# Kernel tuning notes

Measured on AMD Instinct MI355X. Metric: run time of the kernel, lower is better.

## Reference

```python
import jax, jax.numpy as jnp
import numpy as np

X_DIM, Y_DIM = 5, 2
H1, H2 = 560, 40
GRU_H = 5 * (X_DIM * X_DIM + Y_DIM * Y_DIM)  # 145
N_GRU = 2


def _gru_cell(x, h, Wih, Whh, bih, bhh):
    # PyTorch GRUCell math. Wih:(3H,in), Whh:(3H,H)
    gi = Wih @ x + bih
    gh = Whh @ h + bhh
    i_r, i_z, i_n = jnp.split(gi, 3)
    h_r, h_z, h_n = jnp.split(gh, 3)
    r = jax.nn.sigmoid(i_r + h_r)
    z = jax.nn.sigmoid(i_z + h_z)
    n = jnp.tanh(i_n + r * h_n)
    return (1.0 - z) * n + z * h


def setup_inputs() -> dict:
    key = jax.random.key(0)
    ks = jax.random.split(key, 20)
    s = lambda k, sh, fan: (jax.random.uniform(k, sh, jnp.float32, -1.0, 1.0) / np.sqrt(fan))
    inp = {
        "state_inno": jax.random.normal(ks[0], (X_DIM,), jnp.float32),
        "obs_inno": jax.random.normal(ks[1], (Y_DIM,), jnp.float32),
        "diff_state": jax.random.normal(ks[2], (X_DIM,), jnp.float32),
        "diff_obs": jax.random.normal(ks[3], (Y_DIM,), jnp.float32),
        # l1: Linear(14 -> H1)
        "W1": s(ks[4], (H1, 2 * X_DIM + 2 * Y_DIM), 2 * X_DIM + 2 * Y_DIM),
        "b1": s(ks[5], (H1,), 2 * X_DIM + 2 * Y_DIM),
        # GRU layer 0: input H1 -> GRU_H
        "Wih0": s(ks[6], (3 * GRU_H, H1), GRU_H),
        "Whh0": s(ks[7], (3 * GRU_H, GRU_H), GRU_H),
        "bih0": s(ks[8], (3 * GRU_H,), GRU_H),
        "bhh0": s(ks[9], (3 * GRU_H,), GRU_H),
        # GRU layer 1: input GRU_H -> GRU_H
        "Wih1": s(ks[10], (3 * GRU_H, GRU_H), GRU_H),
        "Whh1": s(ks[11], (3 * GRU_H, GRU_H), GRU_H),
        "bih1": s(ks[12], (3 * GRU_H,), GRU_H),
        "bhh1": s(ks[13], (3 * GRU_H,), GRU_H),
        # l2: Linear(GRU_H -> H2) -> ReLU -> Linear(H2 -> x_dim*y_dim)
        "W2a": s(ks[14], (H2, GRU_H), GRU_H),
        "b2a": s(ks[15], (H2,), GRU_H),
        "W2b": s(ks[16], (X_DIM * Y_DIM, H2), H2),
        "b2b": s(ks[17], (X_DIM * Y_DIM,), H2),
        # hidden state hn: (n_layers, batch=1, GRU_H) -> squeeze batch
        "hn": jax.random.normal(ks[18], (N_GRU, GRU_H), jnp.float32),
    }
    return inp


def reference(state_inno, obs_inno, diff_state, diff_obs,
              W1, b1, Wih0, Whh0, bih0, bhh0, Wih1, Whh1, bih1, bhh1,
              W2a, b2a, W2b, b2b, hn):
    x = jnp.concatenate([state_inno, obs_inno, diff_state, diff_obs])  # (14,)
    l1_out = jax.nn.relu(W1 @ x + b1)  # (H1,)
    h0 = _gru_cell(l1_out, hn[0], Wih0, Whh0, bih0, bhh0)  # (GRU_H,)
    h1 = _gru_cell(h0, hn[1], Wih1, Whh1, bih1, bhh1)       # (GRU_H,)
    l2_hidden = jax.nn.relu(W2a @ h1 + b2a)
    l2_out = W2b @ l2_hidden + b2b  # (x_dim*y_dim,)
    kalman_gain = l2_out.reshape(X_DIM, Y_DIM)
    return kalman_gain
```

## Files before the change

kernel.cpp:

```cpp
#include <hip/hip_runtime.h>

#define X_DIM 5
#define Y_DIM 2
#define H1 560
#define H2 40
#define GRUH 145
#define G3 435
#define NB_H0 37
#define NB_GH1 109
#define NB_K2 37

__device__ __forceinline__ float wave_reduce(float v) {
#pragma unroll
    for (int off = 32; off > 0; off >>= 1)
        v += __shfl_xor(v, off, 64);
    return v;
}

__device__ __forceinline__ float sigmoidf_(float x) {
    return 1.0f / (1.0f + __expf(-x));
}

__global__ __launch_bounds__(256) void k1_gru0(
    const float* __restrict__ si, const float* __restrict__ oi,
    const float* __restrict__ dst, const float* __restrict__ dob,
    const float* __restrict__ W1, const float* __restrict__ b1,
    const float* __restrict__ Wih0, const float* __restrict__ Whh0,
    const float* __restrict__ bih0, const float* __restrict__ bhh0,
    const float* __restrict__ Whh1, const float* __restrict__ bhh1,
    const float* __restrict__ hn,
    unsigned* __restrict__ ctr,
    float* __restrict__ h0g, float* __restrict__ gh1g)
{
    __shared__ float sx[14];
    __shared__ __align__(16) float sl1[H1];
    __shared__ float shn[GRUH];

    const int tid = threadIdx.x;
    const int wid = tid >> 6, lane = tid & 63;

    if (blockIdx.x < NB_H0) {
        if (tid < X_DIM)                      sx[tid] = si[tid];
        else if (tid < X_DIM + Y_DIM)         sx[tid] = oi[tid - X_DIM];
        else if (tid < 2 * X_DIM + Y_DIM)     sx[tid] = dst[tid - X_DIM - Y_DIM];
        else if (tid < 2 * X_DIM + 2 * Y_DIM) sx[tid] = dob[tid - 2 * X_DIM - Y_DIM];
        if (tid >= 64 && tid < 64 + GRUH) shn[tid - 64] = hn[tid - 64];
        __syncthreads();

        for (int j = tid; j < H1; j += 256) {
            float a = b1[j];
            const float* wp = W1 + j * 14;
#pragma unroll
            for (int k = 0; k < 14; ++k) a = fmaf(wp[k], sx[k], a);
            sl1[j] = fmaxf(a, 0.0f);
        }
        __syncthreads();

        const int e = blockIdx.x * 4 + wid;
        if (e < GRUH) {
            float a0 = 0.f, a1 = 0.f, a2 = 0.f;
            const float4* r0 = reinterpret_cast<const float4*>(Wih0 + (e           ) * H1);
            const float4* r1 = reinterpret_cast<const float4*>(Wih0 + (e +   GRUH  ) * H1);
            const float4* r2 = reinterpret_cast<const float4*>(Wih0 + (e + 2 * GRUH) * H1);
            for (int k = lane; k * 4 < H1; k += 64) {
                const float4 xv = *reinterpret_cast<const float4*>(&sl1[k * 4]);
                const float4 w0 = r0[k], w1 = r1[k], w2 = r2[k];
                a0 = fmaf(w0.x, xv.x, fmaf(w0.y, xv.y, fmaf(w0.z, xv.z, fmaf(w0.w, xv.w, a0))));
                a1 = fmaf(w1.x, xv.x, fmaf(w1.y, xv.y, fmaf(w1.z, xv.z, fmaf(w1.w, xv.w, a1))));
                a2 = fmaf(w2.x, xv.x, fmaf(w2.y, xv.y, fmaf(w2.z, xv.z, fmaf(w2.w, xv.w, a2))));
            }
            float a3 = 0.f, a4 = 0.f, a5 = 0.f;
            for (int k = lane; k < GRUH; k += 64) {
                const float hv = shn[k];
                a3 = fmaf(Whh0[(e           ) * GRUH + k], hv, a3);
                a4 = fmaf(Whh0[(e +   GRUH  ) * GRUH + k], hv, a4);
                a5 = fmaf(Whh0[(e + 2 * GRUH) * GRUH + k], hv, a5);
            }
            a0 = wave_reduce(a0); a1 = wave_reduce(a1); a2 = wave_reduce(a2);
            a3 = wave_reduce(a3); a4 = wave_reduce(a4); a5 = wave_reduce(a5);
            if (lane == 0) {
                const float r = sigmoidf_(a0 + bih0[e]            + a3 + bhh0[e]);
                const float z = sigmoidf_(a1 + bih0[e + GRUH]     + a4 + bhh0[e + GRUH]);
                const float n = tanhf   (a2 + bih0[e + 2 * GRUH] + r * (a5 + bhh0[e + 2 * GRUH]));
                h0g[e] = (1.0f - z) * n + z * shn[e];
            }
        }
    } else {
        if (blockIdx.x == NB_H0 && tid == 0)
            __hip_atomic_store(ctr, 0u, __ATOMIC_RELAXED, __HIP_MEMORY_SCOPE_AGENT);
        if (tid < GRUH) shn[tid] = hn[GRUH + tid];
        __syncthreads();

        const int r = (blockIdx.x - NB_H0) * 4 + wid;
        if (r < G3) {
            float a = 0.f;
            const float* rp = Whh1 + r * GRUH;
            for (int k = lane; k < GRUH; k += 64)
                a = fmaf(rp[k], shn[k], a);
            a = wave_reduce(a);
            if (lane == 0) gh1g[r] = a + bhh1[r];
        }
    }
}

__global__ __launch_bounds__(256) void k2_gru1_head(
    const float* __restrict__ Wih1, const float* __restrict__ bih1,
    const float* __restrict__ W2a, const float* __restrict__ b2a,
    const float* __restrict__ W2b, const float* __restrict__ b2b,
    const float* __restrict__ hn,
    const float* __restrict__ h0g, const float* __restrict__ gh1g,
    unsigned* __restrict__ ctr,
    float* __restrict__ h1g, float* __restrict__ out)
{
    __shared__ float sh0[GRUH];
    __shared__ float sh1[GRUH];
    __shared__ float sl2h[H2];
    __shared__ unsigned slast;

    const int tid = threadIdx.x;
    const int wid = tid >> 6, lane = tid & 63;
    const int e = blockIdx.x * 4 + wid;

    if (tid < GRUH) sh0[tid] = h0g[tid];
    __syncthreads();

    if (e < GRUH) {
        float c0 = 0.f, c1 = 0.f, c2 = 0.f;
        for (int k = lane; k < GRUH; k += 64) {
            const float hv = sh0[k];
            c0 = fmaf(Wih1[(e           ) * GRUH + k], hv, c0);
            c1 = fmaf(Wih1[(e +   GRUH  ) * GRUH + k], hv, c1);
            c2 = fmaf(Wih1[(e + 2 * GRUH) * GRUH + k], hv, c2);
        }
        c0 = wave_reduce(c0); c1 = wave_reduce(c1); c2 = wave_reduce(c2);
        if (lane == 0) {
            const float r = sigmoidf_(c0 + bih1[e]            + gh1g[e]);
            const float z = sigmoidf_(c1 + bih1[e + GRUH]     + gh1g[e + GRUH]);
            const float n = tanhf   (c2 + bih1[e + 2 * GRUH] + r * gh1g[e + 2 * GRUH]);
            const float v = (1.0f - z) * n + z * hn[GRUH + e];
            __hip_atomic_store(&h1g[e], v, __ATOMIC_RELEASE, __HIP_MEMORY_SCOPE_AGENT);
        }
    }
    __syncthreads();
    if (tid == 0) {
        const unsigned old =
            __hip_atomic_fetch_add(ctr, 1u, __ATOMIC_ACQ_REL, __HIP_MEMORY_SCOPE_AGENT);
        slast = (old == NB_K2 - 1u) ? 1u : 0u;
    }
    __syncthreads();
    if (!slast) return;

    for (int j = tid; j < GRUH; j += 256)
        sh1[j] = __hip_atomic_load(&h1g[j], __ATOMIC_ACQUIRE, __HIP_MEMORY_SCOPE_AGENT);
    __syncthreads();

    for (int row = wid * 2; row < H2; row += 8) {
        float a0 = 0.f, a1 = 0.f;
        const float* rp0 = W2a + row * GRUH;
        const float* rp1 = W2a + (row + 1) * GRUH;
        for (int k = lane; k < GRUH; k += 64) {
            const float hv = sh1[k];
            a0 = fmaf(rp0[k], hv, a0);
            a1 = fmaf(rp1[k], hv, a1);
        }
        a0 = wave_reduce(a0); a1 = wave_reduce(a1);
        if (lane == 0) {
            sl2h[row]     = fmaxf(a0 + b2a[row],     0.0f);
            sl2h[row + 1] = fmaxf(a1 + b2a[row + 1], 0.0f);
        }
    }
    __syncthreads();
    if (tid < X_DIM * Y_DIM) {
        float a = b2b[tid];
        const float* rp = W2b + tid * H2;
#pragma unroll
        for (int k = 0; k < H2; ++k) a = fmaf(rp[k], sl2h[k], a);
        out[tid] = a;
    }
}

extern "C" void kernel_launch(void* const* d_in, const int* in_sizes, int n_in,
                              void* d_out, int out_size, void* d_ws, size_t ws_size,
                              hipStream_t stream) {
    const float* si   = (const float*)d_in[0];
    const float* oi   = (const float*)d_in[1];
    const float* dst  = (const float*)d_in[2];
    const float* dob  = (const float*)d_in[3];
    const float* W1   = (const float*)d_in[4];
    const float* b1   = (const float*)d_in[5];
    const float* Wih0 = (const float*)d_in[6];
    const float* Whh0 = (const float*)d_in[7];
    const float* bih0 = (const float*)d_in[8];
    const float* bhh0 = (const float*)d_in[9];
    const float* Wih1 = (const float*)d_in[10];
    const float* Whh1 = (const float*)d_in[11];
    const float* bih1 = (const float*)d_in[12];
    const float* bhh1 = (const float*)d_in[13];
    const float* W2a  = (const float*)d_in[14];
    const float* b2a  = (const float*)d_in[15];
    const float* W2b  = (const float*)d_in[16];
    const float* b2b  = (const float*)d_in[17];
    const float* hn   = (const float*)d_in[18];

    float* ws = (float*)d_ws;
    unsigned* ctr = (unsigned*)d_ws;
    float* h0g  = ws + 64;
    float* gh1g = ws + 64 + 256;
    float* h1g  = ws + 64 + 256 + 512;

    hipLaunchKernelGGL(k1_gru0, dim3(NB_H0 + NB_GH1), dim3(256), 0, stream,
                       si, oi, dst, dob, W1, b1, Wih0, Whh0, bih0, bhh0,
                       Whh1, bhh1, hn, ctr, h0g, gh1g);
    hipLaunchKernelGGL(k2_gru1_head, dim3(NB_K2), dim3(256), 0, stream,
                       Wih1, bih1, W2a, b2a, W2b, b2b, hn, h0g, gh1g,
                       ctr, h1g, (float*)d_out);
}
```

Baseline: 17.43 us.

## Hoist weight loads into registers before dependent syncs and fully unroll GRU dot products

Every wave now issues all of its weight, bias and hidden-state loads into registers at kernel entry, before the l1 computation, the barrier, or the last-block counter. The GRU and head dot products become fully unrolled register FMAs with clamped row indices. The head weights (W2a, W2b) are prefetched by every block before the completion check. The goal is to overlap global-memory latency with the serial dependency chain, at the cost of more registers and redundant head-weight loads in blocks that then exit.

```diff
diff --git a/kernel.cpp b/kernel.cpp
--- a/kernel.cpp
+++ b/kernel.cpp
@@ -19,6 +19,10 @@
 
 __device__ __forceinline__ float sigmoidf_(float x) {
     return 1.0f / (1.0f + __expf(-x));
+}
+
+__device__ __forceinline__ float dot4(float4 a, float4 b) {
+    return fmaf(a.x, b.x, fmaf(a.y, b.y, fmaf(a.z, b.z, a.w * b.w)));
 }
 
 __global__ __launch_bounds__(256) void k1_gru0(
@@ -32,74 +36,88 @@
     unsigned* __restrict__ ctr,
     float* __restrict__ h0g, float* __restrict__ gh1g)
 {
-    __shared__ float sx[14];
-    __shared__ __align__(16) float sl1[H1];
-    __shared__ float shn[GRUH];
-
     const int tid = threadIdx.x;
     const int wid = tid >> 6, lane = tid & 63;
+    const bool t3 = (lane < 17);
 
     if (blockIdx.x < NB_H0) {
-        if (tid < X_DIM)                      sx[tid] = si[tid];
-        else if (tid < X_DIM + Y_DIM)         sx[tid] = oi[tid - X_DIM];
-        else if (tid < 2 * X_DIM + Y_DIM)     sx[tid] = dst[tid - X_DIM - Y_DIM];
-        else if (tid < 2 * X_DIM + 2 * Y_DIM) sx[tid] = dob[tid - 2 * X_DIM - Y_DIM];
-        if (tid >= 64 && tid < 64 + GRUH) shn[tid - 64] = hn[tid - 64];
-        __syncthreads();
+        __shared__ __align__(16) float sl1[H1];
+        const int e   = blockIdx.x * 4 + wid;
+        const bool act = (e < GRUH);
+        const int ee  = act ? e : (GRUH - 1);
+
+        const float* wr0 = Whh0 + (ee           ) * GRUH;
+        const float* wr1 = Whh0 + (ee +   GRUH  ) * GRUH;
+        const float* wr2 = Whh0 + (ee + 2 * GRUH) * GRUH;
+        const float h_a = hn[lane], h_b = hn[lane + 64], h_c = t3 ? hn[lane + 128] : 0.f;
+        const float w00 = wr0[lane], w01 = wr0[lane + 64], w02 = t3 ? wr0[lane + 128] : 0.f;
+        const float w10 = wr1[lane], w11 = wr1[lane + 64], w12 = t3 ? wr1[lane + 128] : 0.f;
+        const float w20 = wr2[lane], w21 = wr2[lane + 64], w22 = t3 ? wr2[lane + 128] : 0.f;
+
+        const bool f3 = (lane < 12);
+        const float4 z4 = make_float4(0.f, 0.f, 0.f, 0.f);
+        const float4* p0 = reinterpret_cast<const float4*>(Wih0 + (ee           ) * H1);
+        const float4* p1 = reinterpret_cast<const float4*>(Wih0 + (ee +   GRUH  ) * H1);
+        const float4* p2 = reinterpret_cast<const float4*>(Wih0 + (ee + 2 * GRUH) * H1);
+        const float4 q00 = p0[lane], q01 = p0[lane + 64], q02 = f3 ? p0[lane + 128] : z4;
+        const float4 q10 = p1[lane], q11 = p1[lane + 64], q12 = f3 ? p1[lane + 128] : z4;
+        const float4 q20 = p2[lane], q21 = p2[lane + 64], q22 = f3 ? p2[lane + 128] : z4;
+
+        const float bi0 = bih0[ee], bi1 = bih0[ee + GRUH], bi2 = bih0[ee + 2 * GRUH];
+        const float bh0 = bhh0[ee], bh1 = bhh0[ee + GRUH], bh2 = bhh0[ee + 2 * GRUH];
+        const float hne = hn[ee];
+
+        float x[14];
+#pragma unroll
+        for (int k = 0; k < 5; ++k) x[k] = si[k];
+        x[5] = oi[0]; x[6] = oi[1];
+#pragma unroll
+        for (int k = 0; k < 5; ++k) x[7 + k] = dst[k];
+        x[12] = dob[0]; x[13] = dob[1];
 
         for (int j = tid; j < H1; j += 256) {
             float a = b1[j];
             const float* wp = W1 + j * 14;
 #pragma unroll
-            for (int k = 0; k < 14; ++k) a = fmaf(wp[k], sx[k], a);
+            for (int k = 0; k < 14; ++k) a = fmaf(wp[k], x[k], a);
             sl1[j] = fmaxf(a, 0.0f);
         }
+
+        float a3 = fmaf(w00, h_a, fmaf(w01, h_b, w02 * h_c));
+        float a4 = fmaf(w10, h_a, fmaf(w11, h_b, w12 * h_c));
+        float a5 = fmaf(w20, h_a, fmaf(w21, h_b, w22 * h_c));
+
         __syncthreads();
 
-        const int e = blockIdx.x * 4 + wid;
-        if (e < GRUH) {
-            float a0 = 0.f, a1 = 0.f, a2 = 0.f;
-            const float4* r0 = reinterpret_cast<const float4*>(Wih0 + (e           ) * H1);
-            const float4* r1 = reinterpret_cast<const float4*>(Wih0 + (e +   GRUH  ) * H1);
-            const float4* r2 = reinterpret_cast<const float4*>(Wih0 + (e + 2 * GRUH) * H1);
-            for (int k = lane; k * 4 < H1; k += 64) {
-                const float4 xv = *reinterpret_cast<const float4*>(&sl1[k * 4]);
-                const float4 w0 = r0[k], w1 = r1[k], w2 = r2[k];
-                a0 = fmaf(w0.x, xv.x, fmaf(w0.y, xv.y, fmaf(w0.z, xv.z, fmaf(w0.w, xv.w, a0))));
-                a1 = fmaf(w1.x, xv.x, fmaf(w1.y, xv.y, fmaf(w1.z, xv.z, fmaf(w1.w, xv.w, a1))));
-                a2 = fmaf(w2.x, xv.x, fmaf(w2.y, xv.y, fmaf(w2.z, xv.z, fmaf(w2.w, xv.w, a2))));
-            }
-            float a3 = 0.f, a4 = 0.f, a5 = 0.f;
-            for (int k = lane; k < GRUH; k += 64) {
-                const float hv = shn[k];
-                a3 = fmaf(Whh0[(e           ) * GRUH + k], hv, a3);
-                a4 = fmaf(Whh0[(e +   GRUH  ) * GRUH + k], hv, a4);
-                a5 = fmaf(Whh0[(e + 2 * GRUH) * GRUH + k], hv, a5);
-            }
-            a0 = wave_reduce(a0); a1 = wave_reduce(a1); a2 = wave_reduce(a2);
-            a3 = wave_reduce(a3); a4 = wave_reduce(a4); a5 = wave_reduce(a5);
-            if (lane == 0) {
-                const float r = sigmoidf_(a0 + bih0[e]            + a3 + bhh0[e]);
-                const float z = sigmoidf_(a1 + bih0[e + GRUH]     + a4 + bhh0[e + GRUH]);
-                const float n = tanhf   (a2 + bih0[e + 2 * GRUH] + r * (a5 + bhh0[e + 2 * GRUH]));
-                h0g[e] = (1.0f - z) * n + z * shn[e];
-            }
+        const float4 s0 = *reinterpret_cast<const float4*>(&sl1[4 * lane]);
+        const float4 s1 = *reinterpret_cast<const float4*>(&sl1[4 * (lane + 64)]);
+        const float4 s2 = f3 ? *reinterpret_cast<const float4*>(&sl1[4 * (lane + 128)]) : z4;
+        float a0 = dot4(q00, s0) + dot4(q01, s1) + dot4(q02, s2);
+        float a1 = dot4(q10, s0) + dot4(q11, s1) + dot4(q12, s2);
+        float a2 = dot4(q20, s0) + dot4(q21, s1) + dot4(q22, s2);
+
+        a0 = wave_reduce(a0); a1 = wave_reduce(a1); a2 = wave_reduce(a2);
+        a3 = wave_reduce(a3); a4 = wave_reduce(a4); a5 = wave_reduce(a5);
+        if (lane == 0 && act) {
+            const float r = sigmoidf_(a0 + bi0 + a3 + bh0);
+            const float z = sigmoidf_(a1 + bi1 + a4 + bh1);
+            const float n = tanhf   (a2 + bi2 + r * (a5 + bh2));
+            h0g[e] = (1.0f - z) * n + z * hne;
         }
     } else {
         if (blockIdx.x == NB_H0 && tid == 0)
             __hip_atomic_store(ctr, 0u, __ATOMIC_RELAXED, __HIP_MEMORY_SCOPE_AGENT);
-        if (tid < GRUH) shn[tid] = hn[GRUH + tid];
-        __syncthreads();
-
-        const int r = (blockIdx.x - NB_H0) * 4 + wid;
-        if (r < G3) {
-            float a = 0.f;
-            const float* rp = Whh1 + r * GRUH;
-            for (int k = lane; k < GRUH; k += 64)
-                a = fmaf(rp[k], shn[k], a);
-            a = wave_reduce(a);
-            if (lane == 0) gh1g[r] = a + bhh1[r];
-        }
+        const int r   = (blockIdx.x - NB_H0) * 4 + wid;
+        const bool act = (r < G3);
+        const int rr  = act ? r : (G3 - 1);
+        const float* rp = Whh1 + rr * GRUH;
+        const float wa = rp[lane], wb = rp[lane + 64], wc = t3 ? rp[lane + 128] : 0.f;
+        const float ha = hn[GRUH + lane], hb = hn[GRUH + lane + 64],
+                    hc = t3 ? hn[GRUH + lane + 128] : 0.f;
+        const float bb = bhh1[rr];
+        float a = fmaf(wa, ha, fmaf(wb, hb, wc * hc));
+        a = wave_reduce(a);
+        if (lane == 0 && act) gh1g[r] = a + bb;
     }
 }
 
@@ -112,34 +130,39 @@
     unsigned* __restrict__ ctr,
     float* __restrict__ h1g, float* __restrict__ out)
 {
-    __shared__ float sh0[GRUH];
     __shared__ float sh1[GRUH];
     __shared__ float sl2h[H2];
     __shared__ unsigned slast;
 
     const int tid = threadIdx.x;
     const int wid = tid >> 6, lane = tid & 63;
-    const int e = blockIdx.x * 4 + wid;
-
-    if (tid < GRUH) sh0[tid] = h0g[tid];
-    __syncthreads();
-
-    if (e < GRUH) {
-        float c0 = 0.f, c1 = 0.f, c2 = 0.f;
-        for (int k = lane; k < GRUH; k += 64) {
-            const float hv = sh0[k];
-            c0 = fmaf(Wih1[(e           ) * GRUH + k], hv, c0);
-            c1 = fmaf(Wih1[(e +   GRUH  ) * GRUH + k], hv, c1);
-            c2 = fmaf(Wih1[(e + 2 * GRUH) * GRUH + k], hv, c2);
-        }
-        c0 = wave_reduce(c0); c1 = wave_reduce(c1); c2 = wave_reduce(c2);
-        if (lane == 0) {
-            const float r = sigmoidf_(c0 + bih1[e]            + gh1g[e]);
-            const float z = sigmoidf_(c1 + bih1[e + GRUH]     + gh1g[e + GRUH]);
-            const float n = tanhf   (c2 + bih1[e + 2 * GRUH] + r * gh1g[e + 2 * GRUH]);
-            const float v = (1.0f - z) * n + z * hn[GRUH + e];
-            __hip_atomic_store(&h1g[e], v, __ATOMIC_RELEASE, __HIP_MEMORY_SCOPE_AGENT);
-        }
+    const bool t3 = (lane < 17);
+    const int e   = blockIdx.x * 4 + wid;
+    const bool act = (e < GRUH);
+    const int ee  = act ? e : (GRUH - 1);
+
+    const float* r0 = Wih1 + (ee           ) * GRUH;
+    const float* r1 = Wih1 + (ee +   GRUH  ) * GRUH;
+    const float* r2 = Wih1 + (ee + 2 * GRUH) * GRUH;
+    const float w0a = r0[lane], w0b = r0[lane + 64], w0c = t3 ? r0[lane + 128] : 0.f;
+    const float w1a = r1[lane], w1b = r1[lane + 64], w1c = t3 ? r1[lane + 128] : 0.f;
+    const float w2a = r2[lane], w2b = r2[lane + 64], w2c = t3 ? r2[lane + 128] : 0.f;
+    const float g0 = gh1g[ee], g1 = gh1g[ee + GRUH], g2 = gh1g[ee + 2 * GRUH];
+    const float bi0 = bih1[ee], bi1 = bih1[ee + GRUH], bi2 = bih1[ee + 2 * GRUH];
+    const float hne = hn[GRUH + ee];
+
+    const float x0 = h0g[lane], x1 = h0g[lane + 64], x2 = t3 ? h0g[lane + 128] : 0.f;
+
+    float c0 = fmaf(w0a, x0, fmaf(w0b, x1, w0c * x2));
+    float c1 = fmaf(w1a, x0, fmaf(w1b, x1, w1c * x2));
+    float c2 = fmaf(w2a, x0, fmaf(w2b, x1, w2c * x2));
+    c0 = wave_reduce(c0); c1 = wave_reduce(c1); c2 = wave_reduce(c2);
+    if (lane == 0 && act) {
+        const float r = sigmoidf_(c0 + bi0 + g0);
+        const float z = sigmoidf_(c1 + bi1 + g1);
+        const float n = tanhf   (c2 + bi2 + r * g2);
+        const float v = (1.0f - z) * n + z * hne;
+        __hip_atomic_store(&h1g[e], v, __ATOMIC_RELEASE, __HIP_MEMORY_SCOPE_AGENT);
     }
     __syncthreads();
     if (tid == 0) {
@@ -147,6 +170,27 @@
             __hip_atomic_fetch_add(ctr, 1u, __ATOMIC_ACQ_REL, __HIP_MEMORY_SCOPE_AGENT);
         slast = (old == NB_K2 - 1u) ? 1u : 0u;
     }
+
+    float wa[10][3];
+    const int rbase = wid * 10;
+#pragma unroll
+    for (int m = 0; m < 10; ++m) {
+        const float* rp = W2a + (rbase + m) * GRUH;
+        wa[m][0] = rp[lane];
+        wa[m][1] = rp[lane + 64];
+        wa[m][2] = t3 ? rp[lane + 128] : 0.f;
+    }
+    float ba[10];
+#pragma unroll
+    for (int m = 0; m < 10; ++m) ba[m] = b2a[rbase + m];
+    float wb2[H2], bb2 = 0.f;
+    if (tid < X_DIM * Y_DIM) {
+        const float* rp = W2b + tid * H2;
+#pragma unroll
+        for (int k = 0; k < H2; ++k) wb2[k] = rp[k];
+        bb2 = b2b[tid];
+    }
+
     __syncthreads();
     if (!slast) return;
 
@@ -154,27 +198,18 @@
         sh1[j] = __hip_atomic_load(&h1g[j], __ATOMIC_ACQUIRE, __HIP_MEMORY_SCOPE_AGENT);
     __syncthreads();
 
-    for (int row = wid * 2; row < H2; row += 8) {
-        float a0 = 0.f, a1 = 0.f;
-        const float* rp0 = W2a + row * GRUH;
-        const float* rp1 = W2a + (row + 1) * GRUH;
-        for (int k = lane; k < GRUH; k += 64) {
-            const float hv = sh1[k];
-            a0 = fmaf(rp0[k], hv, a0);
-            a1 = fmaf(rp1[k], hv, a1);
-        }
-        a0 = wave_reduce(a0); a1 = wave_reduce(a1);
-        if (lane == 0) {
-            sl2h[row]     = fmaxf(a0 + b2a[row],     0.0f);
-            sl2h[row + 1] = fmaxf(a1 + b2a[row + 1], 0.0f);
-        }
+    const float ya = sh1[lane], yb = sh1[lane + 64], yc = t3 ? sh1[lane + 128] : 0.f;
+#pragma unroll
+    for (int m = 0; m < 10; ++m) {
+        float a = fmaf(wa[m][0], ya, fmaf(wa[m][1], yb, wa[m][2] * yc));
+        a = wave_reduce(a);
+        if (lane == 0) sl2h[rbase + m] = fmaxf(a + ba[m], 0.0f);
     }
     __syncthreads();
     if (tid < X_DIM * Y_DIM) {
-        float a = b2b[tid];
-        const float* rp = W2b + tid * H2;
-#pragma unroll
-        for (int k = 0; k < H2; ++k) a = fmaf(rp[k], sl2h[k], a);
+        float a = bb2;
+#pragma unroll
+        for (int k = 0; k < H2; ++k) a = fmaf(wb2[k], sl2h[k], a);
         out[tid] = a;
     }
 }
```

New measurement: 16.33 us. 6.3% less time.
